# Optimization experiments

Hardware: AMD Instinct MI355X
Metric: run time of the kernel (lower is better)

The kernel has to match this reference:

```python
import jax, jax.numpy as jnp
import numpy as np

N = 102400   # total nodes (256 graphs x 400 nodes)
E = 1600000  # total edges
B = 256      # number of graphs
F_IN = 4
H = 128
GH = 120     # GRU hidden
C_IN = 84
L = 100


def setup_inputs() -> dict:
    key = jax.random.key(0)
    ks = jax.random.split(key, 32)
    rn = lambda k, shape, sc: (jax.random.normal(k, shape, jnp.float32) * sc)
    s = lambda fan: 1.0 / np.sqrt(fan)
    inp = {}
    inp["x"] = rn(ks[0], (N, F_IN), 1.0)
    inp["edge_index"] = jax.random.randint(ks[1], (2, E), 0, N)
    inp["batch"] = jnp.repeat(jnp.arange(B), N // B)  # sorted segment ids, no empty segments
    inp["target01"] = rn(ks[2], (B, C_IN, L), 1.0)
    # GraphConv params: out = segsum(x_j) @ W_rel + b + x @ W_root
    inp["W1_rel"] = rn(ks[3], (F_IN, H), s(F_IN)); inp["W1_root"] = rn(ks[4], (F_IN, H), s(F_IN)); inp["b1"] = jnp.zeros((H,), jnp.float32)
    inp["W2_rel"] = rn(ks[5], (H, H), s(H)); inp["W2_root"] = rn(ks[6], (H, H), s(H)); inp["b2"] = jnp.zeros((H,), jnp.float32)
    inp["W3_rel"] = rn(ks[7], (H, H), s(H)); inp["W3_root"] = rn(ks[8], (H, H), s(H)); inp["b3"] = jnp.zeros((H,), jnp.float32)
    # Conv1d(84 -> 128, k=3)
    inp["Wc"] = rn(ks[9], (H, C_IN, 3), s(C_IN * 3)); inp["bc"] = jnp.zeros((H,), jnp.float32)
    # Bidirectional GRU(128 -> 120)
    inp["Wih_f"] = rn(ks[10], (3 * GH, H), s(H)); inp["Whh_f"] = rn(ks[11], (3 * GH, GH), s(GH))
    inp["bih_f"] = jnp.zeros((3 * GH,), jnp.float32); inp["bhh_f"] = jnp.zeros((3 * GH,), jnp.float32)
    inp["Wih_b"] = rn(ks[12], (3 * GH, H), s(H)); inp["Whh_b"] = rn(ks[13], (3 * GH, GH), s(GH))
    inp["bih_b"] = jnp.zeros((3 * GH,), jnp.float32); inp["bhh_b"] = jnp.zeros((3 * GH,), jnp.float32)
    # Dense head
    inp["Wd1"] = rn(ks[14], (4816, 102), s(4816)); inp["bd1"] = jnp.zeros((102,), jnp.float32)
    inp["Wd3"] = rn(ks[15], (102, 2), s(102)); inp["bd3"] = jnp.zeros((2,), jnp.float32)
    return inp


def _graph_conv(x, src, dst, W_rel, b, W_root, n):
    # PyG GraphConv, aggr='add': lin_rel(sum_j x_j) + lin_root(x)
    agg = jax.ops.segment_sum(x[src], dst, num_segments=n)
    return agg @ W_rel + b + x @ W_root


def _gru_dir(xs, Wih, Whh, bih, bhh, reverse):
    # xs: [T, B, D] -> [T, B, GH]; PyTorch GRU cell equations
    h0 = jnp.zeros((xs.shape[1], Whh.shape[1]), xs.dtype)
    def step(h, xt):
        gi = xt @ Wih.T + bih
        gh = h @ Whh.T + bhh
        ir, iz, i_n = jnp.split(gi, 3, axis=-1)
        hr, hz, h_n = jnp.split(gh, 3, axis=-1)
        r = jax.nn.sigmoid(ir + hr)
        z = jax.nn.sigmoid(iz + hz)
        n = jnp.tanh(i_n + r * h_n)
        h2 = (1.0 - z) * n + z * h
        return h2, h2
    _, ys = jax.lax.scan(step, h0, xs, reverse=reverse)
    return ys


def reference(x, edge_index, batch, target01, W1_rel, W1_root, b1, W2_rel, W2_root, b2,
              W3_rel, W3_root, b3, Wc, bc, Wih_f, Whh_f, bih_f, bhh_f,
              Wih_b, Whh_b, bih_b, bhh_b, Wd1, bd1, Wd3, bd3):
    src, dst = edge_index[0], edge_index[1]
    n = x.shape[0]
    x1 = jax.nn.relu(_graph_conv(x, src, dst, W1_rel, b1, W1_root, n))
    x2 = jax.nn.relu(_graph_conv(x1, src, dst, W2_rel, b2, W2_root, n))
    x3 = jax.nn.relu(_graph_conv(x2, src, dst, W3_rel, b3, W3_root, n)) + x1  # residual
    x4 = jax.nn.relu(_graph_conv(x3, src, dst, W3_rel, b3, W3_root, n))      # conv3 reused
    gmax = jax.ops.segment_max(x4, batch, num_segments=B)
    gsum = jax.ops.segment_sum(x4, batch, num_segments=B)
    cnt = jax.ops.segment_sum(jnp.ones((n, 1), x4.dtype), batch, num_segments=B)
    g = jnp.concatenate([gmax, gsum / cnt], axis=1)  # [B, 256]
    # Conv1d (valid, k=3) + relu
    xl = jax.lax.conv_general_dilated(target01, Wc, (1,), 'VALID',
                                      dimension_numbers=('NCH', 'OIH', 'NCH')) + bc[None, :, None]
    xl = jax.nn.relu(xl)  # [B, 128, 98]
    Lp = (xl.shape[2] // 5) * 5
    xt = xl[:, :, :Lp].reshape(B, H, Lp // 5, 5).mean(-1)  # avg_pool1d k=5 -> [B,128,19]
    xs = jnp.transpose(xt, (2, 0, 1))  # [T, B, 128]
    yf = _gru_dir(xs, Wih_f, Whh_f, bih_f, bhh_f, False)
    yb = _gru_dir(xs, Wih_b, Whh_b, bih_b, bhh_b, True)
    y = jnp.concatenate([yf, yb], axis=-1)            # [T, B, 240]
    y = jnp.transpose(y, (1, 0, 2)).reshape(B, -1)    # [B, 4560]
    xc = jnp.concatenate([g, y], axis=1)              # [B, 4816]
    xc = jax.nn.relu(xc @ Wd1 + bd1)
    return jax.nn.log_softmax(xc @ Wd3 + bd3, axis=-1)
```

## Files before the change

### kernel.cpp

```cpp
#include <hip/hip_runtime.h>
#include <cmath>

constexpr int N_NODES = 102400;
constexpr int N_EDGES = 1600000;
constexpr int BGR     = 256;
constexpr int NPG     = 400;
constexpr int F_IN    = 4;
constexpr int H       = 128;
constexpr int GH      = 120;
constexpr int G3      = 360;
constexpr int C_IN    = 84;
constexpr int LSEQ    = 100;
constexpr int TT      = 19;
constexpr int DHEAD   = 4816;
constexpr int D1O     = 102;
constexpr int KCOMB   = 256;
constexpr int CAP     = 64;
constexpr int NXCD    = 8;
constexpr int NPX     = N_NODES / NXCD;
constexpr int SGRP    = 104;

using short8 = __attribute__((ext_vector_type(8))) short;
using f32x4  = __attribute__((ext_vector_type(4))) float;

__device__ __forceinline__ short f2bf(float f) {
    unsigned u = __float_as_uint(f);
    u += 0x7FFFu + ((u >> 16) & 1u);
    return (short)(u >> 16);
}
__device__ __forceinline__ float bf2f(short s) {
    return __uint_as_float(((unsigned)(unsigned short)s) << 16);
}

__device__ __forceinline__ void tr_seg(const float* __restrict__ in, float* __restrict__ out,
                                       int R, int C, int i) {
    if (i < R * C) {
        int r = i / C, c = i % C;
        out[(long)c * R + r] = in[i];
    }
}
__device__ __forceinline__ void wbt_seg(const float* __restrict__ Wrel, const float* __restrict__ Wroot,
                                        short* __restrict__ WBT, int i) {
    if (i < H * KCOMB) {
        int h = i >> 8, k = i & 255;
        float v = (k < H) ? Wrel[k * H + h] : Wroot[(k - H) * H + h];
        WBT[h * KCOMB + k] = f2bf(v);
    }
}
constexpr int PB0 = 126;
constexpr int PB1 = 180;
constexpr int PB2 = 180;
constexpr int PB3 = 169;
constexpr int PB4 = 169;
constexpr int PB6 = 128;
constexpr int PB7 = 128;
constexpr int PREP_BLOCKS = PB0+PB1+PB2+PB3+PB4+PB6+PB7;

__global__ void prep_fused(const float* Wc, float* WCT,
                           const float* Wihf, float* WIHTF,
                           const float* Wihb, float* WIHTB,
                           const float* Whhf, float* WHHTF,
                           const float* Whhb, float* WHHTB,
                           const float* W2rel, const float* W2root, short* WBT2,
                           const float* W3rel, const float* W3root, short* WBT3) {
    int b = blockIdx.x;
    int t = threadIdx.x;
    if (b < PB0) { tr_seg(Wc,   WCT,   128, 252, b * 256 + t); return; }  b -= PB0;
    if (b < PB1) { tr_seg(Wihf, WIHTF, G3,  H,   b * 256 + t); return; }  b -= PB1;
    if (b < PB2) { tr_seg(Wihb, WIHTB, G3,  H,   b * 256 + t); return; }  b -= PB2;
    if (b < PB3) { tr_seg(Whhf, WHHTF, G3,  GH,  b * 256 + t); return; }  b -= PB3;
    if (b < PB4) { tr_seg(Whhb, WHHTB, G3,  GH,  b * 256 + t); return; }  b -= PB4;
    if (b < PB6) { wbt_seg(W2rel, W2root, WBT2, b * 256 + t); return; }   b -= PB6;
    wbt_seg(W3rel, W3root, WBT3, b * 256 + t);
}

__global__ __launch_bounds__(256) void transpose_tiled(const float* __restrict__ in,
                                                       float* __restrict__ out, int R, int C) {
    __shared__ float tile[32][33];
    const int rb = blockIdx.x * 32, cb = blockIdx.y * 32;
    const int tx = threadIdx.x & 31, ty = threadIdx.x >> 5;
#pragma unroll
    for (int yy = 0; yy < 32; yy += 8) {
        int r = rb + ty + yy, c = cb + tx;
        if (r < R && c < C) tile[ty + yy][tx] = in[(long)r * C + c];
    }
    __syncthreads();
#pragma unroll
    for (int yy = 0; yy < 32; yy += 8) {
        int ro = cb + ty + yy, co = rb + tx;
        if (ro < C && co < R) out[(long)ro * R + co] = tile[tx][ty + yy];
    }
}

__global__ __launch_bounds__(256) void xcd_scatter(const int* __restrict__ src,
                                                   const int* __restrict__ dst,
                                                   int* __restrict__ cnt,
                                                   int* __restrict__ csr, int E) {
    const int g   = blockIdx.x & (NXCD - 1);
    const int grp = blockIdx.x >> 3;
    const int nlo = g * NPX, nhi = nlo + NPX;
    const int stride = SGRP * 256 * 4;
    for (int e = (grp * 256 + threadIdx.x) * 4; e + 3 < E; e += stride) {
        const int4 s = *(const int4*)(src + e);
        const int4 d = *(const int4*)(dst + e);
        if (d.x >= nlo && d.x < nhi) { int p = atomicAdd(&cnt[d.x], 1); csr[((long)d.x << 6) + p] = s.x; }
        if (d.y >= nlo && d.y < nhi) { int p = atomicAdd(&cnt[d.y], 1); csr[((long)d.y << 6) + p] = s.y; }
        if (d.z >= nlo && d.z < nhi) { int p = atomicAdd(&cnt[d.z], 1); csr[((long)d.z << 6) + p] = s.z; }
        if (d.w >= nlo && d.w < nhi) { int p = atomicAdd(&cnt[d.w], 1); csr[((long)d.w << 6) + p] = s.w; }
    }
}

__global__ __launch_bounds__(256) void agg4_csr(const int* __restrict__ cnt,
                                                const int* __restrict__ csr,
                                                const float* __restrict__ x,
                                                float* __restrict__ agg) {
    int i = blockIdx.x * 256 + threadIdx.x;
    int n = i >> 2, c = i & 3;
    const int cn = cnt[n];
    const int* idx = csr + ((long)n << 6);
    float acc = 0.f;
    for (int j = 0; j < cn; ++j) acc += x[(long)idx[j] * 4 + c];
    agg[i] = acc;
}

__global__ void gc1_transform(const float* __restrict__ agg4, const float* __restrict__ x,
                              const float* __restrict__ Wrel, const float* __restrict__ Wroot,
                              const float* __restrict__ bias, float* __restrict__ out,
                              short* __restrict__ outb) {
    long i = (long)blockIdx.x * 256 + threadIdx.x;
    int h = (int)(i & (H - 1));
    long n = i >> 7;
    const float4 a  = *(const float4*)(agg4 + n * 4);
    const float4 xv = *(const float4*)(x    + n * 4);
    float acc = bias[h]
        + a.x  * Wrel[0 * H + h] + a.y  * Wrel[1 * H + h]
        + a.z  * Wrel[2 * H + h] + a.w  * Wrel[3 * H + h]
        + xv.x * Wroot[0 * H + h] + xv.y * Wroot[1 * H + h]
        + xv.z * Wroot[2 * H + h] + xv.w * Wroot[3 * H + h];
    float v = fmaxf(acc, 0.f);
    out[i] = v;
    outb[i] = f2bf(v);
}

__global__ __launch_bounds__(256) void agg128_bf(const int* __restrict__ cnt,
                                                 const int* __restrict__ csr,
                                                 const short* __restrict__ xb,
                                                 short* __restrict__ aggb) {
    const int lane = threadIdx.x & 15;
    const int n = blockIdx.x * 16 + (threadIdx.x >> 4);
    const int cn = cnt[n];
    const int* idx = csr + ((long)n << 6);
    const short* xs = xb + lane * 8;
    float acc[8];
#pragma unroll
    for (int q = 0; q < 8; ++q) acc[q] = 0.f;
    int j = 0;
    for (; j + 7 < cn; j += 8) {
        const int4 i0 = *(const int4*)(idx + j);
        const int4 i1 = *(const int4*)(idx + j + 4);
        const short8 r0 = *(const short8*)(xs + (long)i0.x * H);
        const short8 r1 = *(const short8*)(xs + (long)i0.y * H);
        const short8 r2 = *(const short8*)(xs + (long)i0.z * H);
        const short8 r3 = *(const short8*)(xs + (long)i0.w * H);
        const short8 r4 = *(const short8*)(xs + (long)i1.x * H);
        const short8 r5 = *(const short8*)(xs + (long)i1.y * H);
        const short8 r6 = *(const short8*)(xs + (long)i1.z * H);
        const short8 r7 = *(const short8*)(xs + (long)i1.w * H);
#pragma unroll
        for (int q = 0; q < 8; ++q)
            acc[q] += ((bf2f(r0[q]) + bf2f(r1[q])) + (bf2f(r2[q]) + bf2f(r3[q])))
                    + ((bf2f(r4[q]) + bf2f(r5[q])) + (bf2f(r6[q]) + bf2f(r7[q])));
    }
    for (; j + 3 < cn; j += 4) {
        const int4 ii = *(const int4*)(idx + j);
        const short8 r0 = *(const short8*)(xs + (long)ii.x * H);
        const short8 r1 = *(const short8*)(xs + (long)ii.y * H);
        const short8 r2 = *(const short8*)(xs + (long)ii.z * H);
        const short8 r3 = *(const short8*)(xs + (long)ii.w * H);
#pragma unroll
        for (int q = 0; q < 8; ++q)
            acc[q] += (bf2f(r0[q]) + bf2f(r1[q])) + (bf2f(r2[q]) + bf2f(r3[q]));
    }
    for (; j < cn; ++j) {
        const short8 r0 = *(const short8*)(xs + (long)idx[j] * H);
#pragma unroll
        for (int q = 0; q < 8; ++q) acc[q] += bf2f(r0[q]);
    }
    short8 o;
#pragma unroll
    for (int q = 0; q < 8; ++q) o[q] = f2bf(acc[q]);
    *(short8*)(aggb + (long)n * H + lane * 8) = o;
}

template <int RES, int OUTF, int OUTB>
__global__ __launch_bounds__(256) void gc_mfma(
        const short* __restrict__ aggb, const short* __restrict__ xinb,
        const short* __restrict__ WBT, const float* __restrict__ bias,
        const float* __restrict__ res, float* __restrict__ outf,
        short* __restrict__ outb) {
    const int wid   = threadIdx.x >> 6;
    const int lane  = threadIdx.x & 63;
    const int l15   = lane & 15;
    const int kslot = lane >> 4;
    const long n0   = (long)blockIdx.x * 128 + wid * 32;

    f32x4 acc[2][8];
#pragma unroll
    for (int i = 0; i < 2; ++i)
#pragma unroll
        for (int j = 0; j < 8; ++j) acc[i][j] = (f32x4){0.f, 0.f, 0.f, 0.f};

#pragma unroll
    for (int ks = 0; ks < 8; ++ks) {
        const short* srcb = (ks < 4) ? aggb : xinb;
        const int koff = (ks < 4 ? ks * 32 : (ks - 4) * 32) + kslot * 8;
        short8 afr[2];
#pragma unroll
        for (int rt = 0; rt < 2; ++rt)
            afr[rt] = *(const short8*)(srcb + (n0 + rt * 16 + l15) * H + koff);
        const int kb = ks * 32 + kslot * 8;
        short8 bfr[8];
#pragma unroll
        for (int ct = 0; ct < 8; ++ct)
            bfr[ct] = *(const short8*)(WBT + (long)(ct * 16 + l15) * KCOMB + kb);
#pragma unroll
        for (int rt = 0; rt < 2; ++rt)
#pragma unroll
            for (int ct = 0; ct < 8; ++ct)
                acc[rt][ct] = __builtin_amdgcn_mfma_f32_16x16x32_bf16(
                    afr[rt], bfr[ct], acc[rt][ct], 0, 0, 0);
    }

#pragma unroll
    for (int rt = 0; rt < 2; ++rt) {
        const long rbase = n0 + rt * 16 + kslot * 4;
#pragma unroll
        for (int ct = 0; ct < 8; ++ct) {
            const int h = ct * 16 + l15;
            const float bv = bias[h];
#pragma unroll
            for (int r = 0; r < 4; ++r) {
                const long rowi = rbase + r;
                float v = fmaxf(acc[rt][ct][r] + bv, 0.f);
                if (RES) v += res[rowi * H + h];
                if (OUTF) outf[rowi * H + h] = v;
                if (OUTB) outb[rowi * H + h] = f2bf(v);
            }
        }
    }
}

__global__ __launch_bounds__(512) void pool_kernel(const float* __restrict__ x4, float* __restrict__ xc) {
    int g = blockIdx.x;
    int h = threadIdx.x & 127;
    int part = threadIdx.x >> 7;
    const float* base = x4 + ((long)g * NPG + part * 100) * H + h;
    float mx = -INFINITY, sm = 0.f;
#pragma unroll 4
    for (int i = 0; i < 100; ++i) {
        float v = base[(long)i * H];
        mx = fmaxf(mx, v);
        sm += v;
    }
    __shared__ float smx[4][128], ssm[4][128];
    smx[part][h] = mx; ssm[part][h] = sm;
    __syncthreads();
    if (part == 0) {
        float m = fmaxf(fmaxf(smx[0][h], smx[1][h]), fmaxf(smx[2][h], smx[3][h]));
        float s = ssm[0][h] + ssm[1][h] + ssm[2][h] + ssm[3][h];
        xc[(long)g * DHEAD + h] = m;
        xc[(long)g * DHEAD + H + h] = s * (1.f / NPG);
    }
}

__global__ __launch_bounds__(128) void conv1d_pool(const float* __restrict__ in,
                                                   const float* __restrict__ WcT,
                                                   const float* __restrict__ bc,
                                                   float* __restrict__ xs) {
    int p = blockIdx.x;
    int b = blockIdx.y;
    int o = threadIdx.x;
    __shared__ float sIn[C_IN][8];
    const float* ib = in + (long)b * C_IN * LSEQ;
    for (int idx = threadIdx.x; idx < C_IN * 7; idx += 128) {
        int c = idx / 7, j = idx % 7;
        sIn[c][j] = ib[c * LSEQ + 5 * p + j];
    }
    __syncthreads();
    float a0 = 0, a1 = 0, a2 = 0, a3 = 0, a4 = 0;
    for (int c = 0; c < C_IN; ++c) {
        float i0 = sIn[c][0], i1 = sIn[c][1], i2 = sIn[c][2], i3 = sIn[c][3];
        float i4 = sIn[c][4], i5 = sIn[c][5], i6 = sIn[c][6];
        float w0 = WcT[(c * 3 + 0) * H + o];
        float w1 = WcT[(c * 3 + 1) * H + o];
        float w2 = WcT[(c * 3 + 2) * H + o];
        a0 += w0 * i0 + w1 * i1 + w2 * i2;
        a1 += w0 * i1 + w1 * i2 + w2 * i3;
        a2 += w0 * i2 + w1 * i3 + w2 * i4;
        a3 += w0 * i3 + w1 * i4 + w2 * i5;
        a4 += w0 * i4 + w1 * i5 + w2 * i6;
    }
    float bcv = bc[o];
    float r = fmaxf(a0 + bcv, 0.f) + fmaxf(a1 + bcv, 0.f) + fmaxf(a2 + bcv, 0.f)
            + fmaxf(a3 + bcv, 0.f) + fmaxf(a4 + bcv, 0.f);
    xs[((long)p * BGR + b) * H + o] = r * 0.2f;
}

__global__ __launch_bounds__(384) void gi_gemm(const float* __restrict__ xs,
                                               const float* __restrict__ WihT,
                                               const float* __restrict__ bih,
                                               float* __restrict__ gi) {
    const long r0 = (long)blockIdx.x * 16;
    const int g = threadIdx.x;
    __shared__ __align__(16) float sX[16][H];
    for (int idx = threadIdx.x; idx < 16 * H; idx += 384)
        sX[idx >> 7][idx & (H - 1)] = xs[r0 * H + idx];
    __syncthreads();
    if (g >= G3) return;
    const float bv = bih[g];
    float acc[16];
#pragma unroll
    for (int r = 0; r < 16; ++r) acc[r] = bv;
    for (int k = 0; k < H; k += 4) {
        float w0 = WihT[(k + 0) * G3 + g], w1 = WihT[(k + 1) * G3 + g];
        float w2 = WihT[(k + 2) * G3 + g], w3 = WihT[(k + 3) * G3 + g];
#pragma unroll
        for (int r = 0; r < 16; ++r) {
            float4 xv = *(const float4*)&sX[r][k];
            acc[r] += xv.x * w0 + xv.y * w1 + xv.z * w2 + xv.w * w3;
        }
    }
#pragma unroll
    for (int r = 0; r < 16; ++r)
        gi[(r0 + r) * G3 + g] = acc[r];
}

__device__ __forceinline__ float sigmoidf_(float x) { return 1.f / (1.f + expf(-x)); }

__global__ __launch_bounds__(384) void gru_kernel(
        const float* __restrict__ giF, const float* __restrict__ giB,
        const float* __restrict__ WhhTF, const float* __restrict__ WhhTB,
        const float* __restrict__ bhhF, const float* __restrict__ bhhB,
        float* __restrict__ xc) {
    const int b = blockIdx.x & (BGR - 1);
    const int dir = blockIdx.x >> 8;
    const float* gi   = dir ? giB : giF;
    const float* WhhT = dir ? WhhTB : WhhTF;
    const float* bhh  = dir ? bhhB : bhhF;
    const int g = threadIdx.x;
    const int gc = g < G3 ? g : (G3 - 1);

    float w[GH];
#pragma unroll
    for (int k = 0; k < GH; ++k) w[k] = WhhT[(long)k * G3 + gc];
    const float bh = bhh[gc];

    __shared__ __align__(16) float sh[GH];
    __shared__ float sgh[G3];
    if (g < GH) sh[g] = 0.f;
    __syncthreads();

    for (int tt = 0; tt < TT; ++tt) {
        const int t = dir ? (TT - 1 - tt) : tt;
        float acc = bh;
#pragma unroll
        for (int k4 = 0; k4 < GH / 4; ++k4) {
            float4 hv = *(const float4*)&sh[k4 * 4];
            acc += hv.x * w[k4 * 4] + hv.y * w[k4 * 4 + 1]
                 + hv.z * w[k4 * 4 + 2] + hv.w * w[k4 * 4 + 3];
        }
        if (g < G3) sgh[g] = acc;
        __syncthreads();
        if (g < GH) {
            const float* gib = gi + ((long)t * BGR + b) * G3;
            float r = sigmoidf_(gib[g] + sgh[g]);
            float z = sigmoidf_(gib[GH + g] + sgh[GH + g]);
            float n = tanhf(gib[2 * GH + g] + r * sgh[2 * GH + g]);
            float h2 = (1.f - z) * n + z * sh[g];
            sh[g] = h2;
            xc[(long)b * DHEAD + 256 + t * 240 + dir * GH + g] = h2;
        }
        __syncthreads();
    }
}

__global__ __launch_bounds__(256) void dense1(const float* __restrict__ xc,
                                              const float* __restrict__ Wd1T,
                                              const float* __restrict__ bd1,
                                              float* __restrict__ d1) {
    const int wid  = blockIdx.x * 4 + (threadIdx.x >> 6);
    const int lane = threadIdx.x & 63;
    const int jg = wid % 26;
    const int bg = wid / 26;
    const int j0 = jg * 4, b0 = bg * 8;

    float acc[4][8];
#pragma unroll
    for (int jj = 0; jj < 4; ++jj)
#pragma unroll
        for (int bb = 0; bb < 8; ++bb) acc[jj][bb] = 0.f;

    for (int i = lane; i < DHEAD / 4; i += 64) {
        float4 wv[4], xv[8];
#pragma unroll
        for (int jj = 0; jj < 4; ++jj) {
            int j = j0 + jj; if (j > D1O - 1) j = D1O - 1;
            wv[jj] = *(const float4*)(Wd1T + (long)j * DHEAD + i * 4);
        }
#pragma unroll
        for (int bb = 0; bb < 8; ++bb)
            xv[bb] = *(const float4*)(xc + (long)(b0 + bb) * DHEAD + i * 4);
#pragma unroll
        for (int jj = 0; jj < 4; ++jj)
#pragma unroll
            for (int bb = 0; bb < 8; ++bb)
                acc[jj][bb] += wv[jj].x * xv[bb].x + wv[jj].y * xv[bb].y
                             + wv[jj].z * xv[bb].z + wv[jj].w * xv[bb].w;
    }
#pragma unroll
    for (int m = 32; m >= 1; m >>= 1)
#pragma unroll
        for (int jj = 0; jj < 4; ++jj)
#pragma unroll
            for (int bb = 0; bb < 8; ++bb)
                acc[jj][bb] += __shfl_xor(acc[jj][bb], m, 64);
    if (lane < 32) {
        const int jj = lane >> 3, bb = lane & 7;
        const int j = j0 + jj;
        if (j < D1O)
            d1[(long)(b0 + bb) * D1O + j] = fmaxf(acc[jj][bb] + bd1[j], 0.f);
    }
}

__global__ void final_head(const float* __restrict__ d1, const float* __restrict__ Wd3,
                           const float* __restrict__ bd3, float* __restrict__ out) {
    int b = threadIdx.x;
    if (b >= BGR) return;
    float v0 = bd3[0], v1 = bd3[1];
    for (int k = 0; k < D1O; ++k) {
        float xv = d1[(long)b * D1O + k];
        v0 += xv * Wd3[k * 2 + 0];
        v1 += xv * Wd3[k * 2 + 1];
    }
    float m = fmaxf(v0, v1);
    float lse = m + logf(expf(v0 - m) + expf(v1 - m));
    out[b * 2 + 0] = v0 - lse;
    out[b * 2 + 1] = v1 - lse;
}

extern "C" void kernel_launch(void* const* d_in, const int* in_sizes, int n_in,
                              void* d_out, int out_size, void* d_ws, size_t ws_size,
                              hipStream_t stream) {
    const float* x      = (const float*)d_in[0];
    const int*   ei     = (const int*)d_in[1];
    const float* tgt    = (const float*)d_in[3];
    const float* W1rel  = (const float*)d_in[4];
    const float* W1root = (const float*)d_in[5];
    const float* b1     = (const float*)d_in[6];
    const float* W2rel  = (const float*)d_in[7];
    const float* W2root = (const float*)d_in[8];
    const float* b2     = (const float*)d_in[9];
    const float* W3rel  = (const float*)d_in[10];
    const float* W3root = (const float*)d_in[11];
    const float* b3     = (const float*)d_in[12];
    const float* Wc     = (const float*)d_in[13];
    const float* bc     = (const float*)d_in[14];
    const float* Wih_f  = (const float*)d_in[15];
    const float* Whh_f  = (const float*)d_in[16];
    const float* bih_f  = (const float*)d_in[17];
    const float* bhh_f  = (const float*)d_in[18];
    const float* Wih_b  = (const float*)d_in[19];
    const float* Whh_b  = (const float*)d_in[20];
    const float* bih_b  = (const float*)d_in[21];
    const float* bhh_b  = (const float*)d_in[22];
    const float* Wd1    = (const float*)d_in[23];
    const float* bd1    = (const float*)d_in[24];
    const float* Wd3    = (const float*)d_in[25];
    const float* bd3    = (const float*)d_in[26];

    const int* srcI = ei;
    const int* dstI = ei + N_EDGES;

    float* ws = (float*)d_ws;
    size_t off = 0;
    float* AGG4  = ws + off; off += (size_t)N_NODES * 4;
    float* X1    = ws + off; off += (size_t)N_NODES * H;
    float* XS    = ws + off; off += (size_t)TT * BGR * H;
    float* GIF   = ws + off; off += (size_t)TT * BGR * G3;
    float* GIB   = ws + off; off += (size_t)TT * BGR * G3;
    float* XC    = ws + off; off += (size_t)BGR * DHEAD;
    float* D1    = ws + off; off += (size_t)BGR * D1O + 2;
    float* WCT   = ws + off; off += (size_t)C_IN * 3 * H;
    float* WIHTF = ws + off; off += (size_t)H * G3;
    float* WIHTB = ws + off; off += (size_t)H * G3;
    float* WHHTF = ws + off; off += (size_t)GH * G3;
    float* WHHTB = ws + off; off += (size_t)GH * G3;
    float* WD1T  = ws + off; off += (size_t)DHEAD * D1O;
    off = (off + 3) & ~(size_t)3;
    short* WBT2  = (short*)(ws + off); off += (size_t)H * KCOMB / 2;
    short* WBT3  = (short*)(ws + off); off += (size_t)H * KCOMB / 2;
    short* AGGB  = (short*)(ws + off); off += (size_t)N_NODES * H / 2;
    short* X1B   = (short*)(ws + off); off += (size_t)N_NODES * H / 2;
    short* X2B   = (short*)(ws + off); off += (size_t)N_NODES * H / 2;
    short* X3B   = (short*)(ws + off); off += (size_t)N_NODES * H / 2;
    int* ibase   = (int*)(ws + off);
    int* CNT     = ibase;
    int* CSR     = ibase + N_NODES;

    prep_fused<<<PREP_BLOCKS, 256, 0, stream>>>(Wc, WCT, Wih_f, WIHTF, Wih_b, WIHTB,
                                                Whh_f, WHHTF, Whh_b, WHHTB,
                                                W2rel, W2root, WBT2, W3rel, W3root, WBT3);
    transpose_tiled<<<dim3((DHEAD + 31) / 32, (D1O + 31) / 32), 256, 0, stream>>>(Wd1, WD1T, DHEAD, D1O);

    hipMemsetAsync(CNT, 0, (size_t)N_NODES * sizeof(int), stream);
    xcd_scatter<<<NXCD * SGRP, 256, 0, stream>>>(srcI, dstI, CNT, CSR, N_EDGES);

    agg4_csr<<<(N_NODES * 4) / 256, 256, 0, stream>>>(CNT, CSR, x, AGG4);
    gc1_transform<<<(N_NODES * H) / 256, 256, 0, stream>>>(AGG4, x, W1rel, W1root, b1, X1, X1B);

    agg128_bf<<<N_NODES / 16, 256, 0, stream>>>(CNT, CSR, X1B, AGGB);
    gc_mfma<0, 0, 1><<<N_NODES / 128, 256, 0, stream>>>(AGGB, X1B, WBT2, b2, nullptr, nullptr, X2B);

    agg128_bf<<<N_NODES / 16, 256, 0, stream>>>(CNT, CSR, X2B, AGGB);
    gc_mfma<1, 0, 1><<<N_NODES / 128, 256, 0, stream>>>(AGGB, X2B, WBT3, b3, X1, nullptr, X3B);

    agg128_bf<<<N_NODES / 16, 256, 0, stream>>>(CNT, CSR, X3B, AGGB);
    gc_mfma<0, 1, 0><<<N_NODES / 128, 256, 0, stream>>>(AGGB, X3B, WBT3, b3, nullptr, X1, nullptr);

    pool_kernel<<<BGR, 512, 0, stream>>>(X1, XC);

    conv1d_pool<<<dim3(TT, BGR), 128, 0, stream>>>(tgt, WCT, bc, XS);

    gi_gemm<<<(TT * BGR) / 16, 384, 0, stream>>>(XS, WIHTF, bih_f, GIF);
    gi_gemm<<<(TT * BGR) / 16, 384, 0, stream>>>(XS, WIHTB, bih_b, GIB);

    gru_kernel<<<2 * BGR, 384, 0, stream>>>(GIF, GIB, WHHTF, WHHTB, bhh_f, bhh_b, XC);

    dense1<<<(26 * 32) / 4, 256, 0, stream>>>(XC, WD1T, bd1, D1);
    final_head<<<1, 256, 0, stream>>>(D1, Wd3, bd3, (float*)d_out);
}
```

Before: 709.6 us.

## Co-schedule GRU branch kernels with graph aggregation kernels and split dense1 K

Merges the independent sequence branch (conv1d+pool, input GEMMs, GRU recurrence) into the same launches as the edge scatter, first-layer aggregation and second aggregation, using block-index ranges to run them concurrently. This targets the serial tail of small, low-occupancy GRU kernels by overlapping them with memory-bound graph work. dense1 now splits K in two and accumulates with atomics into a zeroed buffer, with bias and relu moved into final_head. The changes add launch-size coupling and register pressure from the GRU body inside the 384-thread aggregation kernel.

```diff
diff --git a/kernel.cpp b/kernel.cpp
--- a/kernel.cpp
+++ b/kernel.cpp
@@ -92,35 +92,114 @@
     }
 }
 
-__global__ __launch_bounds__(256) void xcd_scatter(const int* __restrict__ src,
-                                                   const int* __restrict__ dst,
-                                                   int* __restrict__ cnt,
-                                                   int* __restrict__ csr, int E) {
-    const int g   = blockIdx.x & (NXCD - 1);
-    const int grp = blockIdx.x >> 3;
-    const int nlo = g * NPX, nhi = nlo + NPX;
-    const int stride = SGRP * 256 * 4;
-    for (int e = (grp * 256 + threadIdx.x) * 4; e + 3 < E; e += stride) {
-        const int4 s = *(const int4*)(src + e);
-        const int4 d = *(const int4*)(dst + e);
-        if (d.x >= nlo && d.x < nhi) { int p = atomicAdd(&cnt[d.x], 1); csr[((long)d.x << 6) + p] = s.x; }
-        if (d.y >= nlo && d.y < nhi) { int p = atomicAdd(&cnt[d.y], 1); csr[((long)d.y << 6) + p] = s.y; }
-        if (d.z >= nlo && d.z < nhi) { int p = atomicAdd(&cnt[d.z], 1); csr[((long)d.z << 6) + p] = s.z; }
-        if (d.w >= nlo && d.w < nhi) { int p = atomicAdd(&cnt[d.w], 1); csr[((long)d.w << 6) + p] = s.w; }
-    }
-}
-
-__global__ __launch_bounds__(256) void agg4_csr(const int* __restrict__ cnt,
-                                                const int* __restrict__ csr,
-                                                const float* __restrict__ x,
-                                                float* __restrict__ agg) {
-    int i = blockIdx.x * 256 + threadIdx.x;
-    int n = i >> 2, c = i & 3;
-    const int cn = cnt[n];
-    const int* idx = csr + ((long)n << 6);
-    float acc = 0.f;
-    for (int j = 0; j < cn; ++j) acc += x[(long)idx[j] * 4 + c];
-    agg[i] = acc;
+constexpr int SCB = NXCD * SGRP;
+constexpr int C1B = (TT * BGR) / 2;
+
+__global__ __launch_bounds__(256) void scatter_conv1d(
+        const int* __restrict__ src, const int* __restrict__ dst,
+        int* __restrict__ cnt, int* __restrict__ csr, int E,
+        const float* __restrict__ tin, const float* __restrict__ WcT,
+        const float* __restrict__ bc, float* __restrict__ xs) {
+    if (blockIdx.x < SCB) {
+        const int g   = blockIdx.x & (NXCD - 1);
+        const int grp = blockIdx.x >> 3;
+        const int nlo = g * NPX, nhi = nlo + NPX;
+        const int stride = SGRP * 256 * 4;
+        for (int e = (grp * 256 + threadIdx.x) * 4; e + 3 < E; e += stride) {
+            const int4 s = *(const int4*)(src + e);
+            const int4 d = *(const int4*)(dst + e);
+            if (d.x >= nlo && d.x < nhi) { int p = atomicAdd(&cnt[d.x], 1); csr[((long)d.x << 6) + p] = s.x; }
+            if (d.y >= nlo && d.y < nhi) { int p = atomicAdd(&cnt[d.y], 1); csr[((long)d.y << 6) + p] = s.y; }
+            if (d.z >= nlo && d.z < nhi) { int p = atomicAdd(&cnt[d.z], 1); csr[((long)d.z << 6) + p] = s.z; }
+            if (d.w >= nlo && d.w < nhi) { int p = atomicAdd(&cnt[d.w], 1); csr[((long)d.w << 6) + p] = s.w; }
+        }
+        return;
+    }
+    __shared__ float sIn[2][C_IN][8];
+    const int half = threadIdx.x >> 7;
+    const int o    = threadIdx.x & 127;
+    const int id   = (blockIdx.x - SCB) * 2 + half;
+    const int p = id / BGR, b = id % BGR;
+    const float* ib = tin + (long)b * C_IN * LSEQ;
+    for (int idx = o; idx < C_IN * 7; idx += 128) {
+        int c = idx / 7, j = idx % 7;
+        sIn[half][c][j] = ib[c * LSEQ + 5 * p + j];
+    }
+    __syncthreads();
+    float a0 = 0, a1 = 0, a2 = 0, a3 = 0, a4 = 0;
+    for (int c = 0; c < C_IN; ++c) {
+        float i0 = sIn[half][c][0], i1 = sIn[half][c][1], i2 = sIn[half][c][2], i3 = sIn[half][c][3];
+        float i4 = sIn[half][c][4], i5 = sIn[half][c][5], i6 = sIn[half][c][6];
+        float w0 = WcT[(c * 3 + 0) * H + o];
+        float w1 = WcT[(c * 3 + 1) * H + o];
+        float w2 = WcT[(c * 3 + 2) * H + o];
+        a0 += w0 * i0 + w1 * i1 + w2 * i2;
+        a1 += w0 * i1 + w1 * i2 + w2 * i3;
+        a2 += w0 * i2 + w1 * i3 + w2 * i4;
+        a3 += w0 * i3 + w1 * i4 + w2 * i5;
+        a4 += w0 * i4 + w1 * i5 + w2 * i6;
+    }
+    float bcv = bc[o];
+    float r = fmaxf(a0 + bcv, 0.f) + fmaxf(a1 + bcv, 0.f) + fmaxf(a2 + bcv, 0.f)
+            + fmaxf(a3 + bcv, 0.f) + fmaxf(a4 + bcv, 0.f);
+    xs[((long)p * BGR + b) * H + o] = r * 0.2f;
+}
+
+constexpr int A4B = (N_NODES * 4 + 383) / 384;
+constexpr int GIB_ = (TT * BGR) / 16;
+
+__device__ __forceinline__ void gi_body(const float* __restrict__ xs,
+                                        const float* __restrict__ WihT,
+                                        const float* __restrict__ bih,
+                                        float* __restrict__ gi, int bid) {
+    const long r0 = (long)bid * 16;
+    const int g = threadIdx.x;
+    __shared__ __align__(16) float sX[16][H];
+    for (int idx = threadIdx.x; idx < 16 * H; idx += 384)
+        sX[idx >> 7][idx & (H - 1)] = xs[r0 * H + idx];
+    __syncthreads();
+    if (g >= G3) return;
+    const float bv = bih[g];
+    float acc[16];
+#pragma unroll
+    for (int r = 0; r < 16; ++r) acc[r] = bv;
+    for (int k = 0; k < H; k += 4) {
+        float w0 = WihT[(k + 0) * G3 + g], w1 = WihT[(k + 1) * G3 + g];
+        float w2 = WihT[(k + 2) * G3 + g], w3 = WihT[(k + 3) * G3 + g];
+#pragma unroll
+        for (int r = 0; r < 16; ++r) {
+            float4 xv = *(const float4*)&sX[r][k];
+            acc[r] += xv.x * w0 + xv.y * w1 + xv.z * w2 + xv.w * w3;
+        }
+    }
+#pragma unroll
+    for (int r = 0; r < 16; ++r)
+        gi[(r0 + r) * G3 + g] = acc[r];
+}
+
+__global__ __launch_bounds__(384) void agg4_gi(
+        const int* __restrict__ cnt, const int* __restrict__ csr,
+        const float* __restrict__ x, float* __restrict__ agg,
+        const float* __restrict__ xs,
+        const float* __restrict__ WihTF, const float* __restrict__ bihF, float* __restrict__ giF,
+        const float* __restrict__ WihTB, const float* __restrict__ bihB, float* __restrict__ giB) {
+    int b = blockIdx.x;
+    if (b < A4B) {
+        int i = b * 384 + threadIdx.x;
+        if (i < N_NODES * 4) {
+            int n = i >> 2, c = i & 3;
+            const int cn = cnt[n];
+            const int* idx = csr + ((long)n << 6);
+            float acc = 0.f;
+            for (int j = 0; j < cn; ++j) acc += x[(long)idx[j] * 4 + c];
+            agg[i] = acc;
+        }
+        return;
+    }
+    b -= A4B;
+    if (b < GIB_) { gi_body(xs, WihTF, bihF, giF, b); return; }
+    b -= GIB_;
+    gi_body(xs, WihTB, bihB, giB, b);
 }
 
 __global__ void gc1_transform(const float* __restrict__ agg4, const float* __restrict__ x,
@@ -142,12 +221,10 @@
     outb[i] = f2bf(v);
 }
 
-__global__ __launch_bounds__(256) void agg128_bf(const int* __restrict__ cnt,
-                                                 const int* __restrict__ csr,
-                                                 const short* __restrict__ xb,
-                                                 short* __restrict__ aggb) {
-    const int lane = threadIdx.x & 15;
-    const int n = blockIdx.x * 16 + (threadIdx.x >> 4);
+__device__ __forceinline__ void agg_body(const int* __restrict__ cnt,
+                                         const int* __restrict__ csr,
+                                         const short* __restrict__ xb,
+                                         short* __restrict__ aggb, int n, int lane) {
     const int cn = cnt[n];
     const int* idx = csr + ((long)n << 6);
     const short* xs = xb + lane * 8;
@@ -192,6 +269,73 @@
     *(short8*)(aggb + (long)n * H + lane * 8) = o;
 }
 
+__global__ __launch_bounds__(256) void agg128_bf(const int* __restrict__ cnt,
+                                                 const int* __restrict__ csr,
+                                                 const short* __restrict__ xb,
+                                                 short* __restrict__ aggb) {
+    agg_body(cnt, csr, xb, aggb, blockIdx.x * 16 + (threadIdx.x >> 4), threadIdx.x & 15);
+}
+
+constexpr int AGB = (N_NODES + 23) / 24;
+
+__device__ __forceinline__ float sigmoidf_(float x) { return 1.f / (1.f + expf(-x)); }
+
+__device__ void gru_body(const float* __restrict__ gi, const float* __restrict__ WhhT,
+                         const float* __restrict__ bhh, float* __restrict__ xc,
+                         int b, int dir) {
+    const int g = threadIdx.x;
+    const int gc = g < G3 ? g : (G3 - 1);
+    float w[GH];
+#pragma unroll
+    for (int k = 0; k < GH; ++k) w[k] = WhhT[(long)k * G3 + gc];
+    const float bh = bhh[gc];
+
+    __shared__ __align__(16) float sh[GH];
+    __shared__ float sgh[G3];
+    if (g < GH) sh[g] = 0.f;
+    __syncthreads();
+
+    for (int tt = 0; tt < TT; ++tt) {
+        const int t = dir ? (TT - 1 - tt) : tt;
+        float acc = bh;
+#pragma unroll
+        for (int k4 = 0; k4 < GH / 4; ++k4) {
+            float4 hv = *(const float4*)&sh[k4 * 4];
+            acc += hv.x * w[k4 * 4] + hv.y * w[k4 * 4 + 1]
+                 + hv.z * w[k4 * 4 + 2] + hv.w * w[k4 * 4 + 3];
+        }
+        if (g < G3) sgh[g] = acc;
+        __syncthreads();
+        if (g < GH) {
+            const float* gib = gi + ((long)t * BGR + b) * G3;
+            float r = sigmoidf_(gib[g] + sgh[g]);
+            float z = sigmoidf_(gib[GH + g] + sgh[GH + g]);
+            float n = tanhf(gib[2 * GH + g] + r * sgh[2 * GH + g]);
+            float h2 = (1.f - z) * n + z * sh[g];
+            sh[g] = h2;
+            xc[(long)b * DHEAD + 256 + t * 240 + dir * GH + g] = h2;
+        }
+        __syncthreads();
+    }
+}
+
+__global__ __launch_bounds__(384) void agg2_gru(
+        const int* __restrict__ cnt, const int* __restrict__ csr,
+        const short* __restrict__ xb, short* __restrict__ aggb,
+        const float* __restrict__ giF, const float* __restrict__ giB,
+        const float* __restrict__ WhhTF, const float* __restrict__ WhhTB,
+        const float* __restrict__ bhhF, const float* __restrict__ bhhB,
+        float* __restrict__ xc) {
+    if (blockIdx.x < AGB) {
+        const int n = blockIdx.x * 24 + (threadIdx.x >> 4);
+        if (n < N_NODES) agg_body(cnt, csr, xb, aggb, n, threadIdx.x & 15);
+        return;
+    }
+    const int bid = blockIdx.x - AGB;
+    const int b = bid & (BGR - 1), dir = bid >> 8;
+    gru_body(dir ? giB : giF, dir ? WhhTB : WhhTF, dir ? bhhB : bhhF, xc, b, dir);
+}
+
 template <int RES, int OUTF, int OUTB>
 __global__ __launch_bounds__(256) void gc_mfma(
         const short* __restrict__ aggb, const short* __restrict__ xinb,
@@ -273,126 +417,17 @@
     }
 }
 
-__global__ __launch_bounds__(128) void conv1d_pool(const float* __restrict__ in,
-                                                   const float* __restrict__ WcT,
-                                                   const float* __restrict__ bc,
-                                                   float* __restrict__ xs) {
-    int p = blockIdx.x;
-    int b = blockIdx.y;
-    int o = threadIdx.x;
-    __shared__ float sIn[C_IN][8];
-    const float* ib = in + (long)b * C_IN * LSEQ;
-    for (int idx = threadIdx.x; idx < C_IN * 7; idx += 128) {
-        int c = idx / 7, j = idx % 7;
-        sIn[c][j] = ib[c * LSEQ + 5 * p + j];
-    }
-    __syncthreads();
-    float a0 = 0, a1 = 0, a2 = 0, a3 = 0, a4 = 0;
-    for (int c = 0; c < C_IN; ++c) {
-        float i0 = sIn[c][0], i1 = sIn[c][1], i2 = sIn[c][2], i3 = sIn[c][3];
-        float i4 = sIn[c][4], i5 = sIn[c][5], i6 = sIn[c][6];
-        float w0 = WcT[(c * 3 + 0) * H + o];
-        float w1 = WcT[(c * 3 + 1) * H + o];
-        float w2 = WcT[(c * 3 + 2) * H + o];
-        a0 += w0 * i0 + w1 * i1 + w2 * i2;
-        a1 += w0 * i1 + w1 * i2 + w2 * i3;
-        a2 += w0 * i2 + w1 * i3 + w2 * i4;
-        a3 += w0 * i3 + w1 * i4 + w2 * i5;
-        a4 += w0 * i4 + w1 * i5 + w2 * i6;
-    }
-    float bcv = bc[o];
-    float r = fmaxf(a0 + bcv, 0.f) + fmaxf(a1 + bcv, 0.f) + fmaxf(a2 + bcv, 0.f)
-            + fmaxf(a3 + bcv, 0.f) + fmaxf(a4 + bcv, 0.f);
-    xs[((long)p * BGR + b) * H + o] = r * 0.2f;
-}
-
-__global__ __launch_bounds__(384) void gi_gemm(const float* __restrict__ xs,
-                                               const float* __restrict__ WihT,
-                                               const float* __restrict__ bih,
-                                               float* __restrict__ gi) {
-    const long r0 = (long)blockIdx.x * 16;
-    const int g = threadIdx.x;
-    __shared__ __align__(16) float sX[16][H];
-    for (int idx = threadIdx.x; idx < 16 * H; idx += 384)
-        sX[idx >> 7][idx & (H - 1)] = xs[r0 * H + idx];
-    __syncthreads();
-    if (g >= G3) return;
-    const float bv = bih[g];
-    float acc[16];
-#pragma unroll
-    for (int r = 0; r < 16; ++r) acc[r] = bv;
-    for (int k = 0; k < H; k += 4) {
-        float w0 = WihT[(k + 0) * G3 + g], w1 = WihT[(k + 1) * G3 + g];
-        float w2 = WihT[(k + 2) * G3 + g], w3 = WihT[(k + 3) * G3 + g];
-#pragma unroll
-        for (int r = 0; r < 16; ++r) {
-            float4 xv = *(const float4*)&sX[r][k];
-            acc[r] += xv.x * w0 + xv.y * w1 + xv.z * w2 + xv.w * w3;
-        }
-    }
-#pragma unroll
-    for (int r = 0; r < 16; ++r)
-        gi[(r0 + r) * G3 + g] = acc[r];
-}
-
-__device__ __forceinline__ float sigmoidf_(float x) { return 1.f / (1.f + expf(-x)); }
-
-__global__ __launch_bounds__(384) void gru_kernel(
-        const float* __restrict__ giF, const float* __restrict__ giB,
-        const float* __restrict__ WhhTF, const float* __restrict__ WhhTB,
-        const float* __restrict__ bhhF, const float* __restrict__ bhhB,
-        float* __restrict__ xc) {
-    const int b = blockIdx.x & (BGR - 1);
-    const int dir = blockIdx.x >> 8;
-    const float* gi   = dir ? giB : giF;
-    const float* WhhT = dir ? WhhTB : WhhTF;
-    const float* bhh  = dir ? bhhB : bhhF;
-    const int g = threadIdx.x;
-    const int gc = g < G3 ? g : (G3 - 1);
-
-    float w[GH];
-#pragma unroll
-    for (int k = 0; k < GH; ++k) w[k] = WhhT[(long)k * G3 + gc];
-    const float bh = bhh[gc];
-
-    __shared__ __align__(16) float sh[GH];
-    __shared__ float sgh[G3];
-    if (g < GH) sh[g] = 0.f;
-    __syncthreads();
-
-    for (int tt = 0; tt < TT; ++tt) {
-        const int t = dir ? (TT - 1 - tt) : tt;
-        float acc = bh;
-#pragma unroll
-        for (int k4 = 0; k4 < GH / 4; ++k4) {
-            float4 hv = *(const float4*)&sh[k4 * 4];
-            acc += hv.x * w[k4 * 4] + hv.y * w[k4 * 4 + 1]
-                 + hv.z * w[k4 * 4 + 2] + hv.w * w[k4 * 4 + 3];
-        }
-        if (g < G3) sgh[g] = acc;
-        __syncthreads();
-        if (g < GH) {
-            const float* gib = gi + ((long)t * BGR + b) * G3;
-            float r = sigmoidf_(gib[g] + sgh[g]);
-            float z = sigmoidf_(gib[GH + g] + sgh[GH + g]);
-            float n = tanhf(gib[2 * GH + g] + r * sgh[2 * GH + g]);
-            float h2 = (1.f - z) * n + z * sh[g];
-            sh[g] = h2;
-            xc[(long)b * DHEAD + 256 + t * 240 + dir * GH + g] = h2;
-        }
-        __syncthreads();
-    }
-}
-
 __global__ __launch_bounds__(256) void dense1(const float* __restrict__ xc,
                                               const float* __restrict__ Wd1T,
-                                              const float* __restrict__ bd1,
                                               float* __restrict__ d1) {
-    const int wid  = blockIdx.x * 4 + (threadIdx.x >> 6);
+    const int wid0 = blockIdx.x * 4 + (threadIdx.x >> 6);
     const int lane = threadIdx.x & 63;
+    const int ks   = wid0 & 1;
+    const int wid  = wid0 >> 1;
     const int jg = wid % 26;
     const int bg = wid / 26;
     const int j0 = jg * 4, b0 = bg * 8;
+    const int i0 = ks * 602, i1 = i0 + 602;
 
     float acc[4][8];
 #pragma unroll
@@ -400,7 +435,7 @@
 #pragma unroll
         for (int bb = 0; bb < 8; ++bb) acc[jj][bb] = 0.f;
 
-    for (int i = lane; i < DHEAD / 4; i += 64) {
+    for (int i = i0 + lane; i < i1; i += 64) {
         float4 wv[4], xv[8];
 #pragma unroll
         for (int jj = 0; jj < 4; ++jj) {
@@ -428,17 +463,18 @@
         const int jj = lane >> 3, bb = lane & 7;
         const int j = j0 + jj;
         if (j < D1O)
-            d1[(long)(b0 + bb) * D1O + j] = fmaxf(acc[jj][bb] + bd1[j], 0.f);
-    }
-}
-
-__global__ void final_head(const float* __restrict__ d1, const float* __restrict__ Wd3,
-                           const float* __restrict__ bd3, float* __restrict__ out) {
+            atomicAdd(&d1[(long)(b0 + bb) * D1O + j], acc[jj][bb]);
+    }
+}
+
+__global__ void final_head(const float* __restrict__ d1, const float* __restrict__ bd1,
+                           const float* __restrict__ Wd3, const float* __restrict__ bd3,
+                           float* __restrict__ out) {
     int b = threadIdx.x;
     if (b >= BGR) return;
     float v0 = bd3[0], v1 = bd3[1];
     for (int k = 0; k < D1O; ++k) {
-        float xv = d1[(long)b * D1O + k];
+        float xv = fmaxf(d1[(long)b * D1O + k] + bd1[k], 0.f);
         v0 += xv * Wd3[k * 2 + 0];
         v1 += xv * Wd3[k * 2 + 1];
     }
@@ -513,12 +549,18 @@
     transpose_tiled<<<dim3((DHEAD + 31) / 32, (D1O + 31) / 32), 256, 0, stream>>>(Wd1, WD1T, DHEAD, D1O);
 
     hipMemsetAsync(CNT, 0, (size_t)N_NODES * sizeof(int), stream);
-    xcd_scatter<<<NXCD * SGRP, 256, 0, stream>>>(srcI, dstI, CNT, CSR, N_EDGES);
-
-    agg4_csr<<<(N_NODES * 4) / 256, 256, 0, stream>>>(CNT, CSR, x, AGG4);
+    hipMemsetAsync(D1, 0, (size_t)BGR * D1O * sizeof(float), stream);
+
+    scatter_conv1d<<<SCB + C1B, 256, 0, stream>>>(srcI, dstI, CNT, CSR, N_EDGES,
+                                                  tgt, WCT, bc, XS);
+
+    agg4_gi<<<A4B + 2 * GIB_, 384, 0, stream>>>(CNT, CSR, x, AGG4, XS,
+                                                WIHTF, bih_f, GIF, WIHTB, bih_b, GIB);
+
     gc1_transform<<<(N_NODES * H) / 256, 256, 0, stream>>>(AGG4, x, W1rel, W1root, b1, X1, X1B);
 
-    agg128_bf<<<N_NODES / 16, 256, 0, stream>>>(CNT, CSR, X1B, AGGB);
+    agg2_gru<<<AGB + 2 * BGR, 384, 0, stream>>>(CNT, CSR, X1B, AGGB, GIF, GIB,
+                                                WHHTF, WHHTB, bhh_f, bhh_b, XC);
     gc_mfma<0, 0, 1><<<N_NODES / 128, 256, 0, stream>>>(AGGB, X1B, WBT2, b2, nullptr, nullptr, X2B);
 
     agg128_bf<<<N_NODES / 16, 256, 0, stream>>>(CNT, CSR, X2B, AGGB);
@@ -529,13 +571,6 @@
 
     pool_kernel<<<BGR, 512, 0, stream>>>(X1, XC);
 
-    conv1d_pool<<<dim3(TT, BGR), 128, 0, stream>>>(tgt, WCT, bc, XS);
-
-    gi_gemm<<<(TT * BGR) / 16, 384, 0, stream>>>(XS, WIHTF, bih_f, GIF);
-    gi_gemm<<<(TT * BGR) / 16, 384, 0, stream>>>(XS, WIHTB, bih_b, GIB);
-
-    gru_kernel<<<2 * BGR, 384, 0, stream>>>(GIF, GIB, WHHTF, WHHTB, bhh_f, bhh_b, XC);
-
-    dense1<<<(26 * 32) / 4, 256, 0, stream>>>(XC, WD1T, bd1, D1);
-    final_head<<<1, 256, 0, stream>>>(D1, Wd3, bd3, (float*)d_out);
-}
+    dense1<<<(26 * 32 * 2) / 4, 256, 0, stream>>>(XC, WD1T, D1);
+    final_head<<<1, 256, 0, stream>>>(D1, bd1, Wd3, bd3, (float*)d_out);
+}
```

New measurement: 679.3 us. -4.3%, faster.
